# Kernel tuning notes

Measured on AMD Instinct MI355X. Metric: run time of the kernel, lower is better.

## Reference

```python
import jax, jax.numpy as jnp
import numpy as np

B, N, E, H = 16, 1024, 128, 8  # batch, num_patches, emb_dim, num_heads
INNER = E * H                   # inner_dim = emb_dim * num_heads = 1024
LN_EPS = 1e-5
NEG_MAX = jnp.finfo(jnp.float32).max  # module uses -finfo.max on the diagonal


def setup_inputs() -> dict:
    key = jax.random.key(0)
    k0, k1, k2 = jax.random.split(key, 3)
    x = jax.random.normal(k0, (B, N, E), dtype=jnp.float32)
    ln_w = jnp.ones((E,), jnp.float32)
    ln_b = jnp.zeros((E,), jnp.float32)
    w_qkv = jax.random.normal(k1, (E, 3 * INNER), jnp.float32) * (E ** -0.5)
    scale = jnp.full((H,), E ** -0.5, jnp.float32)  # learnable per-head LSA scale
    w_proj = jax.random.normal(k2, (INNER, E), jnp.float32) * (INNER ** -0.5)
    b_proj = jnp.zeros((E,), jnp.float32)
    return {"x": x, "ln_w": ln_w, "ln_b": ln_b, "w_qkv": w_qkv,
            "scale": scale, "w_proj": w_proj, "b_proj": b_proj}


def reference(x, ln_w, ln_b, w_qkv, scale, w_proj, b_proj):
    # LayerNorm over emb_dim
    mu = jnp.mean(x, axis=-1, keepdims=True)
    var = jnp.mean(jnp.square(x - mu), axis=-1, keepdims=True)
    xn = (x - mu) * jax.lax.rsqrt(var + LN_EPS) * ln_w + ln_b

    # QKV projection (no bias), chunk into q,k,v of [B,N,INNER]
    qkv = xn @ w_qkv
    q, k, v = jnp.split(qkv, 3, axis=-1)

    # 'b n (h d) -> b h n d' with h = H, d = E
    def to_heads(t):
        return t.reshape(B, N, H, E).transpose(0, 2, 1, 3)
    q, k, v = to_heads(q), to_heads(k), to_heads(v)

    # per-head learnable scale (LSA), then mask diagonal to -max
    dots = jnp.einsum("bhnd,bhmd->bhnm", q, k) * scale[None, :, None, None]
    idx = jnp.arange(N)
    dots = dots.at[:, :, idx, idx].set(-NEG_MAX)

    attn = jax.nn.softmax(dots, axis=-1)  # dropout p=0.0 -> identity
    out = jnp.einsum("bhnm,bhmd->bhnd", attn, v)

    # 'b h n d -> b n (h d)', then output projection (with bias)
    out = out.transpose(0, 2, 1, 3).reshape(B, N, INNER)
    return out @ w_proj + b_proj
```

## Files before the change

### kernel.cpp

```cpp
#include <hip/hip_runtime.h>
#include <hip/hip_bf16.h>

typedef __bf16 bf16x8 __attribute__((ext_vector_type(8)));
typedef _Float16 f16x4 __attribute__((ext_vector_type(4)));
typedef float f32x4 __attribute__((ext_vector_type(4)));

__device__ __forceinline__ unsigned short f2bf(float f) {
  union { __hip_bfloat16 h; unsigned short u; } cv;
  cv.h = __float2bfloat16(f);
  return cv.u;
}
__device__ __forceinline__ unsigned short f2h(float f) {
  union { _Float16 h; unsigned short u; } cv;
  cv.h = (_Float16)f;
  return cv.u;
}

__device__ __forceinline__ bf16x8 ld_frag(const unsigned short* p) {
  bf16x8 v;
  __builtin_memcpy(&v, __builtin_assume_aligned(p, 16), 16);
  return v;
}
__device__ __forceinline__ f16x4 ld_h4(const unsigned short* p) {
  f16x4 v;
  __builtin_memcpy(&v, __builtin_assume_aligned(p, 8), 8);
  return v;
}
__device__ __forceinline__ uint4 ld16(const unsigned short* p) {
  uint4 v;
  __builtin_memcpy(&v, __builtin_assume_aligned(p, 16), 16);
  return v;
}
__device__ __forceinline__ void st16(unsigned short* p, uint4 v) {
  __builtin_memcpy(__builtin_assume_aligned(p, 16), &v, 16);
}
__device__ __forceinline__ void dma16(const unsigned short* g, unsigned short* l) {
  __builtin_amdgcn_global_load_lds((const __attribute__((address_space(1))) void*)g,
                                   (__attribute__((address_space(3))) void*)l, 16, 0, 0);
}

__global__ __launch_bounds__(256) void ln_kernel(const float* __restrict__ x,
                                                 const float* __restrict__ w,
                                                 const float* __restrict__ b,
                                                 unsigned short* __restrict__ xn) {
  int wave = threadIdx.x >> 6;
  int lane = threadIdx.x & 63;
  int row = blockIdx.x * 4 + wave;
  const float* xr = x + (size_t)row * 128;
  float2 v = *reinterpret_cast<const float2*>(xr + lane * 2);
  float s1 = v.x + v.y;
  float s2 = v.x * v.x + v.y * v.y;
#pragma unroll
  for (int off = 32; off > 0; off >>= 1) {
    s1 += __shfl_xor(s1, off, 64);
    s2 += __shfl_xor(s2, off, 64);
  }
  float mu = s1 * (1.0f / 128.0f);
  float var = s2 * (1.0f / 128.0f) - mu * mu;
  float rstd = rsqrtf(var + 1e-5f);
  float a0 = (v.x - mu) * rstd * w[lane * 2] + b[lane * 2];
  float a1 = (v.y - mu) * rstd * w[lane * 2 + 1] + b[lane * 2 + 1];
  unsigned int pk = (unsigned int)f2bf(a0) | ((unsigned int)f2bf(a1) << 16);
  *reinterpret_cast<unsigned int*>(xn + (size_t)row * 128 + lane * 2) = pk;
}

__global__ __launch_bounds__(256) void tcast_kernel(const float* __restrict__ in,
                                                    unsigned short* __restrict__ out,
                                                    int R, int C) {
  __shared__ float tile[32][33];
  int tx = threadIdx.x & 31, ty = threadIdx.x >> 5;
  int c0 = blockIdx.x * 32, r0 = blockIdx.y * 32;
#pragma unroll
  for (int k = 0; k < 4; k++)
    tile[ty + 8 * k][tx] = in[(size_t)(r0 + ty + 8 * k) * C + c0 + tx];
  __syncthreads();
#pragma unroll
  for (int k = 0; k < 4; k++)
    out[(size_t)(c0 + ty + 8 * k) * R + r0 + tx] = f2bf(tile[tx][ty + 8 * k]);
}

__global__ __launch_bounds__(256) void qkv_gemm(const unsigned short* __restrict__ A,
                                                const unsigned short* __restrict__ Bt,
                                                const float* __restrict__ scale,
                                                unsigned short* __restrict__ qk,
                                                unsigned short* __restrict__ Vt) {
  __shared__ unsigned short Al[128 * 72];
  __shared__ unsigned short Bl[128 * 72];
  int t = threadIdx.x;
  int i0 = blockIdx.x * 128, c0 = blockIdx.y * 128;
  int lg = t & 7, rr = t >> 3;
  int w = t >> 6, lane = t & 63, l15 = lane & 15, quad = lane >> 4;
  int wy = (w >> 1) * 64, wx = (w & 1) * 64;
  const f32x4 fz = {0.f, 0.f, 0.f, 0.f};
  f32x4 acc[4][4];
#pragma unroll
  for (int i = 0; i < 4; i++)
#pragma unroll
    for (int j = 0; j < 4; j++) acc[i][j] = fz;

#pragma unroll
  for (int kt = 0; kt < 2; kt++) {
    int k0 = kt * 64;
    uint4 areg[4], breg[4];
#pragma unroll
    for (int p = 0; p < 4; p++)
      areg[p] = ld16(&A[(size_t)(i0 + rr + 32 * p) * 128 + k0 + lg * 8]);
#pragma unroll
    for (int p = 0; p < 4; p++)
      breg[p] = ld16(&Bt[(size_t)(c0 + rr + 32 * p) * 128 + k0 + lg * 8]);
    __syncthreads();
#pragma unroll
    for (int p = 0; p < 4; p++) st16(&Al[(rr + 32 * p) * 72 + lg * 8], areg[p]);
#pragma unroll
    for (int p = 0; p < 4; p++) st16(&Bl[(rr + 32 * p) * 72 + lg * 8], breg[p]);
    __syncthreads();
#pragma unroll
    for (int ks = 0; ks < 2; ks++) {
      bf16x8 af[4], bfr[4];
#pragma unroll
      for (int i = 0; i < 4; i++)
        af[i] = ld_frag(&Al[(wy + 16 * i + l15) * 72 + 32 * ks + quad * 8]);
#pragma unroll
      for (int j = 0; j < 4; j++)
        bfr[j] = ld_frag(&Bl[(wx + 16 * j + l15) * 72 + 32 * ks + quad * 8]);
#pragma unroll
      for (int i = 0; i < 4; i++)
#pragma unroll
        for (int j = 0; j < 4; j++)
          acc[i][j] = __builtin_amdgcn_mfma_f32_16x16x32_bf16(af[i], bfr[j], acc[i][j], 0, 0, 0);
    }
  }
  if (blockIdx.y < 16) {
    float qsc = (blockIdx.y < 8) ? scale[blockIdx.y] : 1.0f;
#pragma unroll
    for (int i = 0; i < 4; i++)
#pragma unroll
      for (int j = 0; j < 4; j++)
#pragma unroll
        for (int r = 0; r < 4; r++) {
          int row = i0 + wy + 16 * i + quad * 4 + r;
          int col = c0 + wx + 16 * j + l15;
          qk[(size_t)row * 2048 + col] = f2bf(acc[i][j][r] * qsc);
        }
  } else {
    int vc0 = (blockIdx.y - 16) * 128;
#pragma unroll
    for (int i = 0; i < 4; i++)
#pragma unroll
      for (int j = 0; j < 4; j++) {
        int vcol = vc0 + wx + 16 * j + l15;
        int hh = vcol >> 7, dd = vcol & 127;
        int row0 = i0 + wy + 16 * i + quad * 4;
        int bb = row0 >> 10, nn = row0 & 1023;
        ushort4 pk;
        pk.x = f2h(acc[i][j][0]); pk.y = f2h(acc[i][j][1]);
        pk.z = f2h(acc[i][j][2]); pk.w = f2h(acc[i][j][3]);
        *reinterpret_cast<ushort4*>(Vt + (size_t)(bb * 8 + hh) * 131072 +
                                    (size_t)dd * 1024 + nn) = pk;
      }
  }
}

__global__ __launch_bounds__(256, 2) void attn_kernel(const unsigned short* __restrict__ qk,
                                                      const unsigned short* __restrict__ Vt,
                                                      unsigned short* __restrict__ aout) {
  __shared__ __align__(16) unsigned short Kl[2][64 * 128];
  __shared__ __align__(16) unsigned short Vl[2][128 * 64];
  int t = threadIdx.x;
  int idx = blockIdx.x;
  int bh = idx & 127, qt = idx >> 7;
  int b = bh >> 3, h = bh & 7;
  int q0 = qt * 128;
  int w = t >> 6, lane = t & 63, l15 = lane & 15, quad = lane >> 4;

  bf16x8 qf[2][4];
  {
    const unsigned short* qb = qk + (size_t)(b * 1024) * 2048 + h * 128;
#pragma unroll
    for (int g = 0; g < 2; g++) {
      const unsigned short* qp = qb + (size_t)(q0 + 32 * w + 16 * g + l15) * 2048;
#pragma unroll
      for (int ks = 0; ks < 4; ks++) qf[g][ks] = ld_frag(qp + 32 * ks + quad * 8);
    }
  }
  const f32x4 fz = {0.f, 0.f, 0.f, 0.f};
  f32x4 o[2][8];
#pragma unroll
  for (int g = 0; g < 2; g++)
#pragma unroll
    for (int i = 0; i < 8; i++) o[g][i] = fz;
  float plsum[2] = {0.f, 0.f};

  const unsigned short* kbase = qk + (size_t)(b * 1024) * 2048 + 1024 + h * 128;
  const unsigned short* vbase = Vt + (size_t)bh * 131072;

  int koff[4], voff[4];
#pragma unroll
  for (int i = 0; i < 4; i++) {
    int c = w * 4 + i;
    int krow = c * 4 + (lane >> 4);
    int kg = ((lane & 15) ^ (krow & 7)) * 8;
    koff[i] = krow * 2048 + kg;
    int vrow = c * 8 + (lane >> 3);
    int vg = ((lane & 7) ^ ((vrow >> 1) & 7)) * 8;
    voff[i] = vrow * 1024 + vg;
  }

#pragma unroll
  for (int i = 0; i < 4; i++) {
    dma16(kbase + koff[i], &Kl[0][(w * 4 + i) * 512]);
    dma16(vbase + voff[i], &Vl[0][(w * 4 + i) * 512]);
  }

  for (int kt = 0; kt < 16; kt++) {
    int k0 = kt * 64;
    __syncthreads();
    {
      int nb = (kt + 1) & 1;
      int kn0 = ((kt + 1) & 15) * 64;
#pragma unroll
      for (int i = 0; i < 4; i++) {
        dma16(kbase + (size_t)kn0 * 2048 + koff[i], &Kl[nb][(w * 4 + i) * 512]);
        dma16(vbase + voff[i] + kn0, &Vl[nb][(w * 4 + i) * 512]);
      }
    }
    const unsigned short* Kc = Kl[kt & 1];
    const unsigned short* Vc = Vl[kt & 1];

#pragma unroll
    for (int ct = 0; ct < 4; ct++) {
      f32x4 acc[2] = {fz, fz};
#pragma unroll
      for (int ks = 0; ks < 4; ks++) {
        bf16x8 kf = ld_frag(&Kc[(16 * ct + l15) * 128 + ((4 * ks + quad) ^ (l15 & 7)) * 8]);
#pragma unroll
        for (int g = 0; g < 2; g++)
          acc[g] = __builtin_amdgcn_mfma_f32_16x16x32_bf16(kf, qf[g][ks], acc[g], 0, 0, 0);
      }
      f16x4 pa[2];
#pragma unroll
      for (int g = 0; g < 2; g++) {
        if ((q0 + 32 * w + 16 * g) == (k0 + 16 * ct)) {
#pragma unroll
          for (int r = 0; r < 4; r++) {
            float p = ((quad * 4 + r) == l15) ? 0.f : __expf(acc[g][r]);
            plsum[g] += p;
            pa[g][r] = (_Float16)p;
          }
        } else {
#pragma unroll
          for (int r = 0; r < 4; r++) {
            float p = __expf(acc[g][r]);
            plsum[g] += p;
            pa[g][r] = (_Float16)p;
          }
        }
      }
#pragma unroll
      for (int c8 = 0; c8 < 8; c8++) {
        f16x4 vf = ld_h4(&Vc[(16 * c8 + l15) * 64 + ((4 * ct + quad) ^ (l15 & 14)) * 4]);
#pragma unroll
        for (int g = 0; g < 2; g++)
          o[g][c8] = __builtin_amdgcn_mfma_f32_16x16x16f16(pa[g], vf, o[g][c8], 0, 0, 0);
      }
    }
  }

#pragma unroll
  for (int g = 0; g < 2; g++) {
    float s = plsum[g];
    s += __shfl_xor(s, 16, 64);
    s += __shfl_xor(s, 32, 64);
#pragma unroll
    for (int r = 0; r < 4; r++) {
      float rs = __shfl(s, (lane & 48) + quad * 4 + r, 64);
      float rl = 1.0f / rs;
      int row = b * 1024 + q0 + 32 * w + 16 * g + quad * 4 + r;
#pragma unroll
      for (int c8 = 0; c8 < 8; c8++) {
        int col = h * 128 + 16 * c8 + l15;
        aout[(size_t)row * 1024 + col] = f2bf(o[g][c8][r] * rl);
      }
    }
  }
}

__global__ __launch_bounds__(256) void proj_gemm(const unsigned short* __restrict__ A,
                                                 const unsigned short* __restrict__ Bt,
                                                 const float* __restrict__ bias,
                                                 float* __restrict__ out) {
  __shared__ unsigned short Al[64 * 136];
  __shared__ unsigned short Bl[64 * 136];
  int t = threadIdx.x;
  int i0 = blockIdx.x * 64, c0 = blockIdx.y * 64;
  int w = t >> 6, lane = t & 63, l15 = lane & 15, quad = lane >> 4;
  int wy = (w >> 1) * 32, wx = (w & 1) * 32;
  const f32x4 fz = {0.f, 0.f, 0.f, 0.f};
  f32x4 acc[2][2];
#pragma unroll
  for (int i = 0; i < 2; i++)
#pragma unroll
    for (int j = 0; j < 2; j++) acc[i][j] = fz;
  int l = t & 15, rr = t >> 4;
  for (int kb = 0; kb < 8; kb++) {
    int k0 = kb * 128;
    uint4 areg[4], breg[4];
#pragma unroll
    for (int p = 0; p < 4; p++)
      areg[p] = ld16(&A[(size_t)(i0 + rr + 16 * p) * 1024 + k0 + l * 8]);
#pragma unroll
    for (int p = 0; p < 4; p++)
      breg[p] = ld16(&Bt[(size_t)(c0 + rr + 16 * p) * 1024 + k0 + l * 8]);
    __syncthreads();
#pragma unroll
    for (int p = 0; p < 4; p++) st16(&Al[(rr + 16 * p) * 136 + l * 8], areg[p]);
#pragma unroll
    for (int p = 0; p < 4; p++) st16(&Bl[(rr + 16 * p) * 136 + l * 8], breg[p]);
    __syncthreads();
#pragma unroll
    for (int ks = 0; ks < 4; ks++) {
      bf16x8 af[2], bfr[2];
#pragma unroll
      for (int i = 0; i < 2; i++)
        af[i] = ld_frag(&Al[(wy + 16 * i + l15) * 136 + 32 * ks + quad * 8]);
#pragma unroll
      for (int j = 0; j < 2; j++)
        bfr[j] = ld_frag(&Bl[(wx + 16 * j + l15) * 136 + 32 * ks + quad * 8]);
#pragma unroll
      for (int i = 0; i < 2; i++)
#pragma unroll
        for (int j = 0; j < 2; j++)
          acc[i][j] = __builtin_amdgcn_mfma_f32_16x16x32_bf16(af[i], bfr[j], acc[i][j], 0, 0, 0);
    }
  }
#pragma unroll
  for (int i = 0; i < 2; i++)
#pragma unroll
    for (int j = 0; j < 2; j++) {
      int col = c0 + wx + 16 * j + l15;
      float bv = bias[col];
#pragma unroll
      for (int r = 0; r < 4; r++) {
        int row = i0 + wy + 16 * i + quad * 4 + r;
        out[(size_t)row * 128 + col] = acc[i][j][r] + bv;
      }
    }
}

extern "C" void kernel_launch(void* const* d_in, const int* in_sizes, int n_in,
                              void* d_out, int out_size, void* d_ws, size_t ws_size,
                              hipStream_t stream) {
  const float* x      = (const float*)d_in[0];
  const float* ln_w   = (const float*)d_in[1];
  const float* ln_b   = (const float*)d_in[2];
  const float* w_qkv  = (const float*)d_in[3];
  const float* scale  = (const float*)d_in[4];
  const float* w_proj = (const float*)d_in[5];
  const float* b_proj = (const float*)d_in[6];
  float* out = (float*)d_out;

  char* ws = (char*)d_ws;
  unsigned short* xn     = (unsigned short*)(ws);
  unsigned short* wqkvT  = (unsigned short*)(ws + 4194304);
  unsigned short* wprojT = (unsigned short*)(ws + 4980736);
  unsigned short* qk     = (unsigned short*)(ws + 5242880);
  unsigned short* Vt     = (unsigned short*)(ws + 72351744);
  unsigned short* aout   = (unsigned short*)(ws + 105906176);

  ln_kernel<<<dim3(4096), dim3(256), 0, stream>>>(x, ln_w, ln_b, xn);
  tcast_kernel<<<dim3(96, 4), dim3(256), 0, stream>>>(w_qkv, wqkvT, 128, 3072);
  tcast_kernel<<<dim3(4, 32), dim3(256), 0, stream>>>(w_proj, wprojT, 1024, 128);
  qkv_gemm<<<dim3(128, 24), dim3(256), 0, stream>>>(xn, wqkvT, scale, qk, Vt);
  attn_kernel<<<dim3(1024), dim3(256), 0, stream>>>(qk, Vt, aout);
  proj_gemm<<<dim3(256, 2), dim3(256), 0, stream>>>(aout, wprojT, b_proj, out);
}
```

Measured before the change: 207.1 us.

## Prefetch GEMM tiles into registers, vectorize QK stores, enlarge attention blocks

The QKV and projection GEMMs now issue the global loads for the next K-slice right after the shared-memory stores, so those loads overlap with the MFMA work. For Q/K blocks the QKV GEMM swaps the MFMA operands, giving a transposed accumulator layout that can be written as 4-wide packed stores instead of scalar ones. The attention kernel moves to 512-thread blocks covering 256 query rows with half as many blocks, so each K/V tile in shared memory serves twice as many queries. The cost is higher register pressure and fewer, larger attention blocks under a tighter launch-bounds register budget.

```diff
diff --git a/kernel.cpp b/kernel.cpp
--- a/kernel.cpp
+++ b/kernel.cpp
@@ -97,23 +97,30 @@
   for (int i = 0; i < 4; i++)
 #pragma unroll
     for (int j = 0; j < 4; j++) acc[i][j] = fz;
+  bool qkblk = (blockIdx.y < 16);
+
+  uint4 areg[4], breg[4];
+#pragma unroll
+  for (int p = 0; p < 4; p++) {
+    areg[p] = ld16(&A[(size_t)(i0 + rr + 32 * p) * 128 + lg * 8]);
+    breg[p] = ld16(&Bt[(size_t)(c0 + rr + 32 * p) * 128 + lg * 8]);
+  }
 
 #pragma unroll
   for (int kt = 0; kt < 2; kt++) {
-    int k0 = kt * 64;
-    uint4 areg[4], breg[4];
-#pragma unroll
-    for (int p = 0; p < 4; p++)
-      areg[p] = ld16(&A[(size_t)(i0 + rr + 32 * p) * 128 + k0 + lg * 8]);
-#pragma unroll
-    for (int p = 0; p < 4; p++)
-      breg[p] = ld16(&Bt[(size_t)(c0 + rr + 32 * p) * 128 + k0 + lg * 8]);
     __syncthreads();
 #pragma unroll
     for (int p = 0; p < 4; p++) st16(&Al[(rr + 32 * p) * 72 + lg * 8], areg[p]);
 #pragma unroll
     for (int p = 0; p < 4; p++) st16(&Bl[(rr + 32 * p) * 72 + lg * 8], breg[p]);
     __syncthreads();
+    if (kt == 0) {
+#pragma unroll
+      for (int p = 0; p < 4; p++) {
+        areg[p] = ld16(&A[(size_t)(i0 + rr + 32 * p) * 128 + 64 + lg * 8]);
+        breg[p] = ld16(&Bt[(size_t)(c0 + rr + 32 * p) * 128 + 64 + lg * 8]);
+      }
+    }
 #pragma unroll
     for (int ks = 0; ks < 2; ks++) {
       bf16x8 af[4], bfr[4];
@@ -123,25 +130,34 @@
 #pragma unroll
       for (int j = 0; j < 4; j++)
         bfr[j] = ld_frag(&Bl[(wx + 16 * j + l15) * 72 + 32 * ks + quad * 8]);
-#pragma unroll
-      for (int i = 0; i < 4; i++)
-#pragma unroll
-        for (int j = 0; j < 4; j++)
-          acc[i][j] = __builtin_amdgcn_mfma_f32_16x16x32_bf16(af[i], bfr[j], acc[i][j], 0, 0, 0);
-    }
-  }
-  if (blockIdx.y < 16) {
+      if (qkblk) {
+#pragma unroll
+        for (int i = 0; i < 4; i++)
+#pragma unroll
+          for (int j = 0; j < 4; j++)
+            acc[i][j] = __builtin_amdgcn_mfma_f32_16x16x32_bf16(bfr[j], af[i], acc[i][j], 0, 0, 0);
+      } else {
+#pragma unroll
+        for (int i = 0; i < 4; i++)
+#pragma unroll
+          for (int j = 0; j < 4; j++)
+            acc[i][j] = __builtin_amdgcn_mfma_f32_16x16x32_bf16(af[i], bfr[j], acc[i][j], 0, 0, 0);
+      }
+    }
+  }
+  if (qkblk) {
     float qsc = (blockIdx.y < 8) ? scale[blockIdx.y] : 1.0f;
 #pragma unroll
     for (int i = 0; i < 4; i++)
 #pragma unroll
-      for (int j = 0; j < 4; j++)
-#pragma unroll
-        for (int r = 0; r < 4; r++) {
-          int row = i0 + wy + 16 * i + quad * 4 + r;
-          int col = c0 + wx + 16 * j + l15;
-          qk[(size_t)row * 2048 + col] = f2bf(acc[i][j][r] * qsc);
-        }
+      for (int j = 0; j < 4; j++) {
+        int row = i0 + wy + 16 * i + l15;
+        int col = c0 + wx + 16 * j + quad * 4;
+        ushort4 pk;
+        pk.x = f2bf(acc[i][j][0] * qsc); pk.y = f2bf(acc[i][j][1] * qsc);
+        pk.z = f2bf(acc[i][j][2] * qsc); pk.w = f2bf(acc[i][j][3] * qsc);
+        *reinterpret_cast<ushort4*>(qk + (size_t)row * 2048 + col) = pk;
+      }
   } else {
     int vc0 = (blockIdx.y - 16) * 128;
 #pragma unroll
@@ -161,7 +177,7 @@
   }
 }
 
-__global__ __launch_bounds__(256, 2) void attn_kernel(const unsigned short* __restrict__ qk,
+__global__ __launch_bounds__(512, 4) void attn_kernel(const unsigned short* __restrict__ qk,
                                                       const unsigned short* __restrict__ Vt,
                                                       unsigned short* __restrict__ aout) {
   __shared__ __align__(16) unsigned short Kl[2][64 * 128];
@@ -170,7 +186,7 @@
   int idx = blockIdx.x;
   int bh = idx & 127, qt = idx >> 7;
   int b = bh >> 3, h = bh & 7;
-  int q0 = qt * 128;
+  int q0 = qt * 256;
   int w = t >> 6, lane = t & 63, l15 = lane & 15, quad = lane >> 4;
 
   bf16x8 qf[2][4];
@@ -194,10 +210,10 @@
   const unsigned short* kbase = qk + (size_t)(b * 1024) * 2048 + 1024 + h * 128;
   const unsigned short* vbase = Vt + (size_t)bh * 131072;
 
-  int koff[4], voff[4];
-#pragma unroll
-  for (int i = 0; i < 4; i++) {
-    int c = w * 4 + i;
+  int koff[2], voff[2];
+#pragma unroll
+  for (int i = 0; i < 2; i++) {
+    int c = w * 2 + i;
     int krow = c * 4 + (lane >> 4);
     int kg = ((lane & 15) ^ (krow & 7)) * 8;
     koff[i] = krow * 2048 + kg;
@@ -207,9 +223,9 @@
   }
 
 #pragma unroll
-  for (int i = 0; i < 4; i++) {
-    dma16(kbase + koff[i], &Kl[0][(w * 4 + i) * 512]);
-    dma16(vbase + voff[i], &Vl[0][(w * 4 + i) * 512]);
+  for (int i = 0; i < 2; i++) {
+    dma16(kbase + koff[i], &Kl[0][(w * 2 + i) * 512]);
+    dma16(vbase + voff[i], &Vl[0][(w * 2 + i) * 512]);
   }
 
   for (int kt = 0; kt < 16; kt++) {
@@ -219,9 +235,9 @@
       int nb = (kt + 1) & 1;
       int kn0 = ((kt + 1) & 15) * 64;
 #pragma unroll
-      for (int i = 0; i < 4; i++) {
-        dma16(kbase + (size_t)kn0 * 2048 + koff[i], &Kl[nb][(w * 4 + i) * 512]);
-        dma16(vbase + voff[i] + kn0, &Vl[nb][(w * 4 + i) * 512]);
+      for (int i = 0; i < 2; i++) {
+        dma16(kbase + (size_t)kn0 * 2048 + koff[i], &Kl[nb][(w * 2 + i) * 512]);
+        dma16(vbase + voff[i] + kn0, &Vl[nb][(w * 2 + i) * 512]);
       }
     }
     const unsigned short* Kc = Kl[kt & 1];
@@ -302,21 +318,28 @@
 #pragma unroll
     for (int j = 0; j < 2; j++) acc[i][j] = fz;
   int l = t & 15, rr = t >> 4;
+
+  uint4 areg[4], breg[4];
+#pragma unroll
+  for (int p = 0; p < 4; p++) {
+    areg[p] = ld16(&A[(size_t)(i0 + rr + 16 * p) * 1024 + l * 8]);
+    breg[p] = ld16(&Bt[(size_t)(c0 + rr + 16 * p) * 1024 + l * 8]);
+  }
   for (int kb = 0; kb < 8; kb++) {
-    int k0 = kb * 128;
-    uint4 areg[4], breg[4];
-#pragma unroll
-    for (int p = 0; p < 4; p++)
-      areg[p] = ld16(&A[(size_t)(i0 + rr + 16 * p) * 1024 + k0 + l * 8]);
-#pragma unroll
-    for (int p = 0; p < 4; p++)
-      breg[p] = ld16(&Bt[(size_t)(c0 + rr + 16 * p) * 1024 + k0 + l * 8]);
     __syncthreads();
 #pragma unroll
     for (int p = 0; p < 4; p++) st16(&Al[(rr + 16 * p) * 136 + l * 8], areg[p]);
 #pragma unroll
     for (int p = 0; p < 4; p++) st16(&Bl[(rr + 16 * p) * 136 + l * 8], breg[p]);
     __syncthreads();
+    if (kb < 7) {
+      int k0 = (kb + 1) * 128;
+#pragma unroll
+      for (int p = 0; p < 4; p++) {
+        areg[p] = ld16(&A[(size_t)(i0 + rr + 16 * p) * 1024 + k0 + l * 8]);
+        breg[p] = ld16(&Bt[(size_t)(c0 + rr + 16 * p) * 1024 + k0 + l * 8]);
+      }
+    }
 #pragma unroll
     for (int ks = 0; ks < 4; ks++) {
       bf16x8 af[2], bfr[2];
@@ -371,6 +394,6 @@
   tcast_kernel<<<dim3(96, 4), dim3(256), 0, stream>>>(w_qkv, wqkvT, 128, 3072);
   tcast_kernel<<<dim3(4, 32), dim3(256), 0, stream>>>(w_proj, wprojT, 1024, 128);
   qkv_gemm<<<dim3(128, 24), dim3(256), 0, stream>>>(xn, wqkvT, scale, qk, Vt);
-  attn_kernel<<<dim3(1024), dim3(256), 0, stream>>>(qk, Vt, aout);
+  attn_kernel<<<dim3(512), dim3(512), 0, stream>>>(qk, Vt, aout);
   proj_gemm<<<dim3(256, 2), dim3(256), 0, stream>>>(aout, wprojT, b_proj, out);
 }
```

New measurement: 299.4 us. 44.6% more time.

## Merge prologue kernels, vectorize QK stores via swapped MFMA, use exp2 softmax

Applied to the files above, without the earlier changes.

Folds the LayerNorm and the two weight transpose-cast kernels into one prologue launch, which removes two kernel launches. In the QKV GEMM, the Q/K blocks swap the MFMA operand order so each lane holds four consecutive columns, letting it write them with one 8-byte store instead of four scattered 2-byte stores. The Q scale is premultiplied by log2(e) so the attention kernel can use exp2f in place of __expf. The exp2f change relies on the compiler lowering it to the fast hardware exp2 instruction.

```diff
diff --git a/kernel.cpp b/kernel.cpp
--- a/kernel.cpp
+++ b/kernel.cpp
@@ -39,37 +39,52 @@
                                    (__attribute__((address_space(3))) void*)l, 16, 0, 0);
 }
 
-__global__ __launch_bounds__(256) void ln_kernel(const float* __restrict__ x,
-                                                 const float* __restrict__ w,
-                                                 const float* __restrict__ b,
-                                                 unsigned short* __restrict__ xn) {
-  int wave = threadIdx.x >> 6;
-  int lane = threadIdx.x & 63;
-  int row = blockIdx.x * 4 + wave;
-  const float* xr = x + (size_t)row * 128;
-  float2 v = *reinterpret_cast<const float2*>(xr + lane * 2);
-  float s1 = v.x + v.y;
-  float s2 = v.x * v.x + v.y * v.y;
-#pragma unroll
-  for (int off = 32; off > 0; off >>= 1) {
-    s1 += __shfl_xor(s1, off, 64);
-    s2 += __shfl_xor(s2, off, 64);
-  }
-  float mu = s1 * (1.0f / 128.0f);
-  float var = s2 * (1.0f / 128.0f) - mu * mu;
-  float rstd = rsqrtf(var + 1e-5f);
-  float a0 = (v.x - mu) * rstd * w[lane * 2] + b[lane * 2];
-  float a1 = (v.y - mu) * rstd * w[lane * 2 + 1] + b[lane * 2 + 1];
-  unsigned int pk = (unsigned int)f2bf(a0) | ((unsigned int)f2bf(a1) << 16);
-  *reinterpret_cast<unsigned int*>(xn + (size_t)row * 128 + lane * 2) = pk;
-}
-
-__global__ __launch_bounds__(256) void tcast_kernel(const float* __restrict__ in,
-                                                    unsigned short* __restrict__ out,
-                                                    int R, int C) {
+__global__ __launch_bounds__(256) void prolog_kernel(const float* __restrict__ x,
+                                                     const float* __restrict__ lw,
+                                                     const float* __restrict__ lb,
+                                                     const float* __restrict__ w_qkv,
+                                                     const float* __restrict__ w_proj,
+                                                     unsigned short* __restrict__ xn,
+                                                     unsigned short* __restrict__ wqkvT,
+                                                     unsigned short* __restrict__ wprojT) {
   __shared__ float tile[32][33];
+  int idx = blockIdx.x;
+  if (idx < 4096) {
+    int wave = threadIdx.x >> 6;
+    int lane = threadIdx.x & 63;
+    int row = idx * 4 + wave;
+    const float* xr = x + (size_t)row * 128;
+    float2 v = *reinterpret_cast<const float2*>(xr + lane * 2);
+    float s1 = v.x + v.y;
+    float s2 = v.x * v.x + v.y * v.y;
+#pragma unroll
+    for (int off = 32; off > 0; off >>= 1) {
+      s1 += __shfl_xor(s1, off, 64);
+      s2 += __shfl_xor(s2, off, 64);
+    }
+    float mu = s1 * (1.0f / 128.0f);
+    float var = s2 * (1.0f / 128.0f) - mu * mu;
+    float rstd = rsqrtf(var + 1e-5f);
+    float a0 = (v.x - mu) * rstd * lw[lane * 2] + lb[lane * 2];
+    float a1 = (v.y - mu) * rstd * lw[lane * 2 + 1] + lb[lane * 2 + 1];
+    unsigned int pk = (unsigned int)f2bf(a0) | ((unsigned int)f2bf(a1) << 16);
+    *reinterpret_cast<unsigned int*>(xn + (size_t)row * 128 + lane * 2) = pk;
+    return;
+  }
+  const float* in;
+  unsigned short* out;
+  int R, C, cb, rb;
+  if (idx < 4480) {
+    int rem = idx - 4096;
+    in = w_qkv; out = wqkvT; R = 128; C = 3072;
+    cb = rem % 96; rb = rem / 96;
+  } else {
+    int rem = idx - 4480;
+    in = w_proj; out = wprojT; R = 1024; C = 128;
+    cb = rem % 4; rb = rem / 4;
+  }
   int tx = threadIdx.x & 31, ty = threadIdx.x >> 5;
-  int c0 = blockIdx.x * 32, r0 = blockIdx.y * 32;
+  int c0 = cb * 32, r0 = rb * 32;
 #pragma unroll
   for (int k = 0; k < 4; k++)
     tile[ty + 8 * k][tx] = in[(size_t)(r0 + ty + 8 * k) * C + c0 + tx];
@@ -97,6 +112,7 @@
   for (int i = 0; i < 4; i++)
 #pragma unroll
     for (int j = 0; j < 4; j++) acc[i][j] = fz;
+  bool qkblk = (blockIdx.y < 16);
 
 #pragma unroll
   for (int kt = 0; kt < 2; kt++) {
@@ -123,25 +139,34 @@
 #pragma unroll
       for (int j = 0; j < 4; j++)
         bfr[j] = ld_frag(&Bl[(wx + 16 * j + l15) * 72 + 32 * ks + quad * 8]);
-#pragma unroll
-      for (int i = 0; i < 4; i++)
-#pragma unroll
-        for (int j = 0; j < 4; j++)
-          acc[i][j] = __builtin_amdgcn_mfma_f32_16x16x32_bf16(af[i], bfr[j], acc[i][j], 0, 0, 0);
-    }
-  }
-  if (blockIdx.y < 16) {
-    float qsc = (blockIdx.y < 8) ? scale[blockIdx.y] : 1.0f;
+      if (qkblk) {
+#pragma unroll
+        for (int i = 0; i < 4; i++)
+#pragma unroll
+          for (int j = 0; j < 4; j++)
+            acc[i][j] = __builtin_amdgcn_mfma_f32_16x16x32_bf16(bfr[j], af[i], acc[i][j], 0, 0, 0);
+      } else {
+#pragma unroll
+        for (int i = 0; i < 4; i++)
+#pragma unroll
+          for (int j = 0; j < 4; j++)
+            acc[i][j] = __builtin_amdgcn_mfma_f32_16x16x32_bf16(af[i], bfr[j], acc[i][j], 0, 0, 0);
+      }
+    }
+  }
+  if (qkblk) {
+    float qsc = (blockIdx.y < 8) ? scale[blockIdx.y] * 1.44269504f : 1.0f;
 #pragma unroll
     for (int i = 0; i < 4; i++)
 #pragma unroll
-      for (int j = 0; j < 4; j++)
-#pragma unroll
-        for (int r = 0; r < 4; r++) {
-          int row = i0 + wy + 16 * i + quad * 4 + r;
-          int col = c0 + wx + 16 * j + l15;
-          qk[(size_t)row * 2048 + col] = f2bf(acc[i][j][r] * qsc);
-        }
+      for (int j = 0; j < 4; j++) {
+        int row = i0 + wy + 16 * i + l15;
+        int col = c0 + wx + 16 * j + quad * 4;
+        ushort4 pk;
+        pk.x = f2bf(acc[i][j][0] * qsc); pk.y = f2bf(acc[i][j][1] * qsc);
+        pk.z = f2bf(acc[i][j][2] * qsc); pk.w = f2bf(acc[i][j][3] * qsc);
+        *reinterpret_cast<ushort4*>(qk + (size_t)row * 2048 + col) = pk;
+      }
   } else {
     int vc0 = (blockIdx.y - 16) * 128;
 #pragma unroll
@@ -243,14 +268,14 @@
         if ((q0 + 32 * w + 16 * g) == (k0 + 16 * ct)) {
 #pragma unroll
           for (int r = 0; r < 4; r++) {
-            float p = ((quad * 4 + r) == l15) ? 0.f : __expf(acc[g][r]);
+            float p = ((quad * 4 + r) == l15) ? 0.f : exp2f(acc[g][r]);
             plsum[g] += p;
             pa[g][r] = (_Float16)p;
           }
         } else {
 #pragma unroll
           for (int r = 0; r < 4; r++) {
-            float p = __expf(acc[g][r]);
+            float p = exp2f(acc[g][r]);
             plsum[g] += p;
             pa[g][r] = (_Float16)p;
           }
@@ -367,9 +392,8 @@
   unsigned short* Vt     = (unsigned short*)(ws + 72351744);
   unsigned short* aout   = (unsigned short*)(ws + 105906176);
 
-  ln_kernel<<<dim3(4096), dim3(256), 0, stream>>>(x, ln_w, ln_b, xn);
-  tcast_kernel<<<dim3(96, 4), dim3(256), 0, stream>>>(w_qkv, wqkvT, 128, 3072);
-  tcast_kernel<<<dim3(4, 32), dim3(256), 0, stream>>>(w_proj, wprojT, 1024, 128);
+  prolog_kernel<<<dim3(4608), dim3(256), 0, stream>>>(x, ln_w, ln_b, w_qkv, w_proj,
+                                                      xn, wqkvT, wprojT);
   qkv_gemm<<<dim3(128, 24), dim3(256), 0, stream>>>(xn, wqkvT, scale, qk, Vt);
   attn_kernel<<<dim3(1024), dim3(256), 0, stream>>>(qk, Vt, aout);
   proj_gemm<<<dim3(256, 2), dim3(256), 0, stream>>>(aout, wprojT, b_proj, out);
```

Measured after the change: 220.6 us. +6.5%, slower.
